# Performance work log

Hardware: AMD Instinct MI355X
Metric: run time of the kernel (lower is better)

## Reference

```python
import jax, jax.numpy as jnp
import numpy as np

EPS_IN = 1e-5   # InstanceNorm2d default eps
EPS_VAR = 1e-6  # clamp on attention variance

def instance_norm(x):
    # x: (b, c, h, w); affine=False, biased variance over spatial dims
    mean = jnp.mean(x, axis=(2, 3), keepdims=True)
    var = jnp.var(x, axis=(2, 3), keepdims=True)
    return (x - mean) * jax.lax.rsqrt(var + EPS_IN)

def setup_inputs() -> dict:
    key = jax.random.key(0)
    k1, k2, k3, k4 = jax.random.split(key, 4)
    shp = (4, 512, 64, 64)
    return {
        "c_x": jax.random.normal(k1, shp, dtype=jnp.float32),
        "s_x": jax.random.normal(k2, shp, dtype=jnp.float32),
        "c_1x": jax.random.normal(k3, shp, dtype=jnp.float32),
        "s_1x": jax.random.normal(k4, shp, dtype=jnp.float32),
    }

def reference(c_x, s_x, c_1x, s_1x):
    b, v_dim, h, w = c_x.shape
    hw = h * w
    # Q: (b, hw, qk), K: (b, qk, hw), V: (b, hw, v)
    Q = instance_norm(c_1x).reshape(b, -1, hw).transpose(0, 2, 1)
    K = instance_norm(s_1x).reshape(b, -1, s_1x.shape[2] * s_1x.shape[3])
    V = s_x.reshape(b, v_dim, -1).transpose(0, 2, 1)
    # attention over spatial tokens
    A = jax.nn.softmax(jnp.einsum('bqc,bck->bqk', Q, K), axis=-1)
    M = jnp.einsum('bqk,bkv->bqv', A, V)              # weighted mean
    Var = jnp.einsum('bqk,bkv->bqv', A, V * V) - M * M  # weighted variance
    S = jnp.sqrt(jnp.clip(Var, EPS_VAR, None))
    # back to (b, v, h, w)
    M = M.reshape(b, h, w, -1).transpose(0, 3, 1, 2)
    S = S.reshape(b, h, w, -1).transpose(0, 3, 1, 2)
    return S * instance_norm(c_x) + M
```

## Files before the change

### kernel.cpp

```cpp
#include <hip/hip_runtime.h>
#include <cmath>


#define B_  4
#define C_  512
#define HW_ 4096

typedef _Float16 f16;
typedef _Float16 f16x8 __attribute__((ext_vector_type(8)));
typedef float    f32x4 __attribute__((ext_vector_type(4)));

__device__ __forceinline__ f32x4 mfma16(f16x8 a, f16x8 b, f32x4 c) {
  return __builtin_amdgcn_mfma_f32_16x16x32_f16(a, b, c, 0, 0, 0);
}
__device__ __forceinline__ void g2l16(const f16* g, f16* l) {
  __builtin_amdgcn_global_load_lds(
      (const __attribute__((address_space(1))) void*)g,
      (__attribute__((address_space(3))) void*)l, 16, 0, 0);
}

__global__ __launch_bounds__(256) void k_stats(
    const float* __restrict__ cx, const float* __restrict__ c1,
    const float* __restrict__ s1,
    float2* __restrict__ cxs, float2* __restrict__ c1s, float2* __restrict__ s1s) {
  int c = blockIdx.x, b = blockIdx.y, t = blockIdx.z;
  const float* src = (t == 0 ? cx : (t == 1 ? c1 : s1)) + (size_t)(b * C_ + c) * HW_;
  float s = 0.f, q = 0.f;
  const float4* src4 = (const float4*)src;
  for (int i = threadIdx.x; i < HW_ / 4; i += 256) {
    float4 v = src4[i];
    s += v.x + v.y + v.z + v.w;
    q += v.x * v.x + v.y * v.y + v.z * v.z + v.w * v.w;
  }
#pragma unroll
  for (int off = 1; off < 64; off <<= 1) {
    s += __shfl_xor(s, off);
    q += __shfl_xor(q, off);
  }
  __shared__ float ss[4], sq[4];
  int wv = threadIdx.x >> 6;
  if ((threadIdx.x & 63) == 0) { ss[wv] = s; sq[wv] = q; }
  __syncthreads();
  if (threadIdx.x == 0) {
    float S = ss[0] + ss[1] + ss[2] + ss[3];
    float Q = sq[0] + sq[1] + sq[2] + sq[3];
    float mean = S * (1.f / HW_);
    float var = Q * (1.f / HW_) - mean * mean;
    float2 r;
    r.x = mean;
    r.y = rsqrtf(var + 1e-5f);
    (t == 0 ? cxs : (t == 1 ? c1s : s1s))[b * C_ + c] = r;
  }
}

__global__ __launch_bounds__(256) void k_prept(
    const float* __restrict__ src, const float2* __restrict__ st,
    f16* __restrict__ dst) {
  int pb = blockIdx.x * 64, cb = blockIdx.y * 64, b = blockIdx.z;
  __shared__ float t[64][65];
  int tj = threadIdx.x & 63, tr = threadIdx.x >> 6;
#pragma unroll 4
  for (int p = 0; p < 16; ++p) {
    int cl = p * 4 + tr;
    float2 mr = st[b * C_ + cb + cl];
    float v = src[(size_t)(b * C_ + cb + cl) * HW_ + pb + tj];
    t[cl][tj] = (v - mr.x) * mr.y;
  }
  __syncthreads();
#pragma unroll 4
  for (int p = 0; p < 16; ++p) {
    int pr = p * 4 + tr;
    dst[(size_t)(b * HW_ + pb + pr) * C_ + cb + tj] = (f16)t[tj][pr];
  }
}

__global__ __launch_bounds__(256) void k_prepv(const float* __restrict__ src,
                                               f16* __restrict__ dst) {
  int gid = blockIdx.x * 256 + threadIdx.x;
  const float4* s = (const float4*)src + (size_t)gid * 2;
  float4 v0 = s[0], v1 = s[1];
  f16x8 v = {(f16)v0.x, (f16)v0.y, (f16)v0.z, (f16)v0.w,
             (f16)v1.x, (f16)v1.y, (f16)v1.z, (f16)v1.w};
  *(f16x8*)(dst + (size_t)gid * 8) = v;
}

__global__ __launch_bounds__(256, 2) void k_qk(
    const f16* __restrict__ Qt, const f16* __restrict__ Kt,
    f16* __restrict__ E, float2* __restrict__ mlpart,
    int qspan, int qt128, int npair) {
  int id = blockIdx.x, pair, kt;
  if ((npair & 7) == 0) {
    int xcd = id & 7, j = id >> 3, qrs = npair >> 3;
    pair = xcd * qrs + (j % qrs);
    kt = j / qrs;
  } else {
    pair = id >> 4;
    kt = id & 15;
  }
  int bz = pair / qt128, qt = pair - bz * qt128;

  const f16* Aq = Qt + ((size_t)(bz * qspan + qt * 128)) * C_;
  const f16* Bk = Kt + (size_t)bz * HW_ * C_ + (size_t)kt * 256 * C_;
  f16* Eb = E + ((size_t)(bz * qspan + qt * 128)) * HW_ + kt * 256;
  float2* mlb = mlpart + ((size_t)(bz * qspan + qt * 128)) * 16 + kt;

  __shared__ __align__(16) union ShQK {
    struct { f16 As[128 * 32]; f16 Bs[256 * 32]; } s;
    f16 ebuf[32 * 272];
  } sh;
  __shared__ float sred[2][128];
  f16* As = sh.s.As;
  f16* Bs = sh.s.Bs;

  int t = threadIdx.x, wave = t >> 6, lane = t & 63, lq = lane & 15, quad = lane >> 4;
  int wy = wave >> 1, wx = wave & 1;
  int srow = t >> 2, scol = (t & 3) * 8;

  f32x4 acc[4][8];
#pragma unroll
  for (int mt = 0; mt < 4; ++mt)
#pragma unroll
    for (int nt = 0; nt < 8; ++nt) acc[mt][nt] = (f32x4){0, 0, 0, 0};

  for (int kc = 0; kc < 16; ++kc) {
    __syncthreads();
    g2l16(Aq + (size_t)srow * C_ + kc * 32 + scol, As + t * 8);
    g2l16(Aq + (size_t)(srow + 64) * C_ + kc * 32 + scol, As + 2048 + t * 8);
#pragma unroll
    for (int i = 0; i < 4; ++i)
      g2l16(Bk + (size_t)(srow + 64 * i) * C_ + kc * 32 + scol,
            Bs + i * 2048 + t * 8);
    __syncthreads();
    f16x8 af[4], bf[8];
#pragma unroll
    for (int mt = 0; mt < 4; ++mt)
      af[mt] = *(const f16x8*)(As + (wy * 64 + mt * 16 + lq) * 32 + quad * 8);
#pragma unroll
    for (int nt = 0; nt < 8; ++nt)
      bf[nt] = *(const f16x8*)(Bs + (wx * 128 + nt * 16 + lq) * 32 + quad * 8);
#pragma unroll
    for (int mt = 0; mt < 4; ++mt)
#pragma unroll
      for (int nt = 0; nt < 8; ++nt)
        acc[mt][nt] = mfma16(af[mt], bf[nt], acc[mt][nt]);
  }

#pragma unroll
  for (int mt = 0; mt < 4; ++mt)
#pragma unroll
    for (int r = 0; r < 4; ++r) {
      float v = -1e30f;
#pragma unroll
      for (int nt = 0; nt < 8; ++nt) v = fmaxf(v, acc[mt][nt][r]);
#pragma unroll
      for (int msk = 1; msk < 16; msk <<= 1) v = fmaxf(v, __shfl_xor(v, msk));
      if (lq == 0) sred[wx][wy * 64 + mt * 16 + quad * 4 + r] = v;
    }
  __syncthreads();
  float mrow[4][4];
#pragma unroll
  for (int mt = 0; mt < 4; ++mt)
#pragma unroll
    for (int r = 0; r < 4; ++r) {
      int rr = wy * 64 + mt * 16 + quad * 4 + r;
      mrow[mt][r] = fmaxf(sred[0][rr], sred[1][rr]);
    }

  float rsum[4][4];
#pragma unroll
  for (int mt = 0; mt < 4; ++mt)
#pragma unroll
    for (int r = 0; r < 4; ++r) rsum[mt][r] = 0.f;

#pragma unroll
  for (int mt = 0; mt < 4; ++mt) {
    __syncthreads();
#pragma unroll
    for (int nt = 0; nt < 8; ++nt) {
      f32x4 v = acc[mt][nt];
#pragma unroll
      for (int r = 0; r < 4; ++r) {
        float e = __expf(v[r] - mrow[mt][r]);
        rsum[mt][r] += e;
        sh.ebuf[(wy * 16 + quad * 4 + r) * 272 + wx * 128 + nt * 16 + lq] = (f16)e;
      }
    }
    __syncthreads();
#pragma unroll
    for (int i = 0; i < 4; ++i) {
      int idx = i * 256 + t;
      int rl = idx >> 5, cs = (idx & 31) * 8;
      f16x8 v8 = *(const f16x8*)(sh.ebuf + rl * 272 + cs);
      int grow = (rl >> 4) * 64 + mt * 16 + (rl & 15);
      *(f16x8*)(Eb + (size_t)grow * HW_ + cs) = v8;
    }
  }

#pragma unroll
  for (int mt = 0; mt < 4; ++mt)
#pragma unroll
    for (int r = 0; r < 4; ++r) {
      float v = rsum[mt][r];
#pragma unroll
      for (int msk = 1; msk < 16; msk <<= 1) v += __shfl_xor(v, msk);
      if (lq == 0) sred[wx][wy * 64 + mt * 16 + quad * 4 + r] = v;
    }
  __syncthreads();
  if (wx == 0 && lq == 0) {
#pragma unroll
    for (int mt = 0; mt < 4; ++mt)
#pragma unroll
      for (int r = 0; r < 4; ++r) {
        int rr = wy * 64 + mt * 16 + quad * 4 + r;
        mlb[(size_t)rr * 16] = make_float2(mrow[mt][r], sred[0][rr] + sred[1][rr]);
      }
  }
}

__global__ __launch_bounds__(256) void k_red(const float2* __restrict__ mlpart,
                                             float* __restrict__ alpha) {
  int row = blockIdx.x * 256 + threadIdx.x;
  const float2* p = mlpart + (size_t)row * 16;
  float2 loc[16];
  float m = -1e30f;
#pragma unroll
  for (int i = 0; i < 16; ++i) {
    loc[i] = p[i];
    m = fmaxf(m, loc[i].x);
  }
  float l = 0.f;
#pragma unroll
  for (int i = 0; i < 16; ++i) l += loc[i].y * __expf(loc[i].x - m);
  float invl = 1.f / l;
#pragma unroll
  for (int i = 0; i < 16; ++i)
    alpha[(size_t)row * 16 + i] = __expf(loc[i].x - m) * invl;
}

__global__ __launch_bounds__(256, 2) void k_pv(
    const f16* __restrict__ P, const float* __restrict__ alphaG,
    const f16* __restrict__ V, const float* __restrict__ cx,
    const float2* __restrict__ cxs, float* __restrict__ out,
    int qspan, int qbase, int qt128) {
  int npairs = (int)gridDim.x >> 2;
  int id = blockIdx.x, pair, ct;
  if ((npairs & 7) == 0) {
    int x = id & 7, j = id >> 3, ppx = npairs >> 3;
    pair = x * ppx + (j >> 2);
    ct = j & 3;
  } else {
    pair = id >> 2;
    ct = id & 3;
  }
  int bz = pair / qt128, qt = pair - bz * qt128;

  const f16* Ap = P + ((size_t)(bz * qspan + qt * 128)) * HW_;
  const f16* Bv = V + ((size_t)(bz * C_ + ct * 128)) * HW_;

  __shared__ __align__(16) f16 As[128 * 32], Bs[128 * 32];
  __shared__ float Al[128 * 17];

  int t = threadIdx.x, wave = t >> 6, lane = t & 63, lq = lane & 15, quad = lane >> 4;
  int wy = wave >> 1, wx = wave & 1;
  int srow = t >> 2, scol = (t & 3) * 8;

  {
    const float* ag = alphaG + ((size_t)(bz * qspan + qt * 128)) * 16;
#pragma unroll
    for (int i = 0; i < 8; ++i) {
      int e = i * 256 + t;
      Al[(e >> 4) * 17 + (e & 15)] = ag[e];
    }
  }

  f32x4 accM[4][4], accM2[4][4];
#pragma unroll
  for (int mt = 0; mt < 4; ++mt)
#pragma unroll
    for (int nt = 0; nt < 4; ++nt) {
      accM[mt][nt] = (f32x4){0, 0, 0, 0};
      accM2[mt][nt] = (f32x4){0, 0, 0, 0};
    }

  for (int kc = 0; kc < 128; ++kc) {
    __syncthreads();
    g2l16(Ap + (size_t)srow * HW_ + kc * 32 + scol, As + t * 8);
    g2l16(Ap + (size_t)(srow + 64) * HW_ + kc * 32 + scol, As + 2048 + t * 8);
    g2l16(Bv + (size_t)srow * HW_ + kc * 32 + scol, Bs + t * 8);
    g2l16(Bv + (size_t)(srow + 64) * HW_ + kc * 32 + scol, Bs + 2048 + t * 8);
    __syncthreads();

    int ktl = kc >> 3;
    f16x8 af[4], bf[4], bf2[4];
#pragma unroll
    for (int mt = 0; mt < 4; ++mt) {
      af[mt] = *(const f16x8*)(As + (wy * 64 + mt * 16 + lq) * 32 + quad * 8);
      f16 a = (f16)Al[(wy * 64 + mt * 16 + lq) * 17 + ktl];
      af[mt] = af[mt] * a;
    }
#pragma unroll
    for (int nt = 0; nt < 4; ++nt) {
      bf[nt] = *(const f16x8*)(Bs + (wx * 64 + nt * 16 + lq) * 32 + quad * 8);
      bf2[nt] = bf[nt] * bf[nt];
    }
#pragma unroll
    for (int mt = 0; mt < 4; ++mt)
#pragma unroll
      for (int nt = 0; nt < 4; ++nt) {
        accM[mt][nt] = mfma16(af[mt], bf[nt], accM[mt][nt]);
        accM2[mt][nt] = mfma16(af[mt], bf2[nt], accM2[mt][nt]);
      }
  }

  int chbase = ct * 128 + wx * 64;
#pragma unroll
  for (int mt = 0; mt < 4; ++mt) {
    int q0 = qbase + qt * 128 + wy * 64 + mt * 16 + quad * 4;
#pragma unroll
    for (int nt = 0; nt < 4; ++nt) {
      int c = chbase + nt * 16 + lq;
      float2 st = cxs[bz * C_ + c];
      size_t base = ((size_t)bz * C_ + c) * HW_ + q0;
      float4 cv = *(const float4*)(cx + base);
      f32x4 m1 = accM[mt][nt], m2 = accM2[mt][nt];
      float4 o;
      o.x = sqrtf(fmaxf(m2[0] - m1[0] * m1[0], 1e-6f)) * ((cv.x - st.x) * st.y) + m1[0];
      o.y = sqrtf(fmaxf(m2[1] - m1[1] * m1[1], 1e-6f)) * ((cv.y - st.x) * st.y) + m1[1];
      o.z = sqrtf(fmaxf(m2[2] - m1[2] * m1[2], 1e-6f)) * ((cv.z - st.x) * st.y) + m1[2];
      o.w = sqrtf(fmaxf(m2[3] - m1[3] * m1[3], 1e-6f)) * ((cv.w - st.x) * st.y) + m1[3];
      *(float4*)(out + base) = o;
    }
  }
}

extern "C" void kernel_launch(void* const* d_in, const int* in_sizes, int n_in,
                              void* d_out, int out_size, void* d_ws,
                              size_t ws_size, hipStream_t stream) {
  const float* c_x = (const float*)d_in[0];
  const float* s_x = (const float*)d_in[1];
  const float* c1x = (const float*)d_in[2];
  const float* s1x = (const float*)d_in[3];
  float* out = (float*)d_out;

  char* ws = (char*)d_ws;
  size_t o = 0;
  f16* Qt = (f16*)(ws + o);  o += (size_t)B_ * HW_ * C_ * 2;
  f16* Kt = (f16*)(ws + o);  o += (size_t)B_ * HW_ * C_ * 2;
  f16* Vh = (f16*)(ws + o);  o += (size_t)B_ * HW_ * C_ * 2;
  float2* cxs = (float2*)(ws + o); o += B_ * C_ * sizeof(float2);
  float2* c1s = (float2*)(ws + o); o += B_ * C_ * sizeof(float2);
  float2* s1s = (float2*)(ws + o); o += B_ * C_ * sizeof(float2);
  size_t fixed = (o + 255) & ~(size_t)255;

  const size_t per_row = (size_t)HW_ * 2 + 16 * 8 + 16 * 4;
  struct Cfg { int nb, qs; };
  const Cfg cfgs[5] = {{4, 4096}, {1, 4096}, {1, 2048}, {1, 1024}, {1, 512}};
  Cfg cfg = cfgs[4];
  for (int i = 0; i < 5; ++i) {
    size_t rows = (size_t)cfgs[i].nb * cfgs[i].qs;
    if (fixed + rows * per_row <= ws_size) { cfg = cfgs[i]; break; }
  }
  const int nb = cfg.nb, qspan = cfg.qs, qt128 = qspan / 128;
  const int npair = nb * qt128;
  const size_t rows = (size_t)nb * qspan;
  f16* E = (f16*)(ws + fixed);
  float2* mlpart = (float2*)(ws + fixed + rows * HW_ * 2);
  float* alpha = (float*)(ws + fixed + rows * HW_ * 2 + rows * 16 * 8);

  k_stats<<<dim3(C_, B_, 3), 256, 0, stream>>>(c_x, c1x, s1x, cxs, c1s, s1s);
  k_prept<<<dim3(HW_ / 64, C_ / 64, B_), 256, 0, stream>>>(c1x, c1s, Qt);
  k_prept<<<dim3(HW_ / 64, C_ / 64, B_), 256, 0, stream>>>(s1x, s1s, Kt);
  k_prepv<<<dim3(B_ * C_ * HW_ / 8 / 256), 256, 0, stream>>>(s_x, Vh);

  for (int b0 = 0; b0 < B_; b0 += nb) {
    for (int qb = 0; qb < HW_; qb += qspan) {
      const f16* Qtp = Qt + ((size_t)b0 * HW_ + qb) * C_;
      const f16* Ktp = Kt + (size_t)b0 * HW_ * C_;
      const f16* Vp = Vh + (size_t)b0 * C_ * HW_;
      const float* cxp = c_x + (size_t)b0 * C_ * HW_;
      const float2* cxsp = cxs + b0 * C_;
      float* outp = out + (size_t)b0 * C_ * HW_;

      k_qk<<<dim3((unsigned)(npair * 16)), 256, 0, stream>>>(
          Qtp, Ktp, E, mlpart, qspan, qt128, npair);
      k_red<<<dim3((unsigned)(rows / 256)), 256, 0, stream>>>(mlpart, alpha);
      k_pv<<<dim3((unsigned)(npair * 4)), 256, 0, stream>>>(
          E, alpha, Vp, cxp, cxsp, outp, qspan, qb, qt128);
    }
  }
}
```

Measured before the change: 428.3 us.

## Restructure PV kernel with 256x128 tiles, triple-buffered LDS and swizzle

The PV GEMM kernel moves from 128x128 tiles with 256 threads and a synchronous single-buffer K=32 loop to 256x128 tiles with 512 threads. It uses a three-stage LDS ring with K=64 steps and XOR-swizzled LDS layout. Global-to-LDS loads for stage s+2 are interleaved with MFMA phases under explicit barriers, waitcnts and setprio. Alpha is stored in LDS as fp16. The aim is to hide global load latency, cut bank conflicts and halve P/V refetching, in exchange for much higher LDS use per block, which may reduce occupancy.

```diff
diff --git a/kernel.cpp b/kernel.cpp
--- a/kernel.cpp
+++ b/kernel.cpp
@@ -237,11 +237,63 @@
     alpha[(size_t)row * 16 + i] = __expf(loc[i].x - m) * invl;
 }
 
-__global__ __launch_bounds__(256, 2) void k_pv(
+#define PV_STAGE_A(i)                                                         \
+  g2l16(Ap + (size_t)((i)*64 + srow) * HW_ + s2 * 64 + scol,                  \
+        sm + pnOff + (i)*4096 + t * 8)
+#define PV_STAGE_B(i)                                                         \
+  g2l16(Bv + (size_t)((i)*64 + srow) * HW_ + s2 * 64 + scol,                  \
+        sm + pnOff + 16384 + (i)*4096 + t * 8)
+
+#define PV_PHASE(MH, NH, STAGE_STMT, POST_STMT)                               \
+  {                                                                           \
+    f16x8 af00 = *(const f16x8*)(As_s + aoff + ((MH)*2+0)*1024 + cx0);        \
+    f16x8 af01 = *(const f16x8*)(As_s + aoff + ((MH)*2+0)*1024 + cx1);        \
+    f16x8 af10 = *(const f16x8*)(As_s + aoff + ((MH)*2+1)*1024 + cx0);        \
+    f16x8 af11 = *(const f16x8*)(As_s + aoff + ((MH)*2+1)*1024 + cx1);        \
+    f16x8 bf00 = *(const f16x8*)(Bs_s + boff + ((NH)*2+0)*1024 + cx0);        \
+    f16x8 bf01 = *(const f16x8*)(Bs_s + boff + ((NH)*2+0)*1024 + cx1);        \
+    f16x8 bf10 = *(const f16x8*)(Bs_s + boff + ((NH)*2+1)*1024 + cx0);        \
+    f16x8 bf11 = *(const f16x8*)(Bs_s + boff + ((NH)*2+1)*1024 + cx1);        \
+    STAGE_STMT;                                                               \
+    __builtin_amdgcn_s_barrier();                                             \
+    asm volatile("s_waitcnt lgkmcnt(0)" ::: "memory");                        \
+    __builtin_amdgcn_sched_barrier(0);                                        \
+    __builtin_amdgcn_s_setprio(1);                                            \
+    af00 *= aal[(MH)*2+0]; af01 *= aal[(MH)*2+0];                             \
+    af10 *= aal[(MH)*2+1]; af11 *= aal[(MH)*2+1];                             \
+    {                                                                         \
+      f16x8 b2;                                                               \
+      b2 = bf00 * bf00;                                                       \
+      accM [(MH)*2+0][(NH)*2+0] = mfma16(af00, bf00, accM [(MH)*2+0][(NH)*2+0]); \
+      accM2[(MH)*2+0][(NH)*2+0] = mfma16(af00, b2,   accM2[(MH)*2+0][(NH)*2+0]); \
+      accM [(MH)*2+1][(NH)*2+0] = mfma16(af10, bf00, accM [(MH)*2+1][(NH)*2+0]); \
+      accM2[(MH)*2+1][(NH)*2+0] = mfma16(af10, b2,   accM2[(MH)*2+1][(NH)*2+0]); \
+      b2 = bf10 * bf10;                                                       \
+      accM [(MH)*2+0][(NH)*2+1] = mfma16(af00, bf10, accM [(MH)*2+0][(NH)*2+1]); \
+      accM2[(MH)*2+0][(NH)*2+1] = mfma16(af00, b2,   accM2[(MH)*2+0][(NH)*2+1]); \
+      accM [(MH)*2+1][(NH)*2+1] = mfma16(af10, bf10, accM [(MH)*2+1][(NH)*2+1]); \
+      accM2[(MH)*2+1][(NH)*2+1] = mfma16(af10, b2,   accM2[(MH)*2+1][(NH)*2+1]); \
+      b2 = bf01 * bf01;                                                       \
+      accM [(MH)*2+0][(NH)*2+0] = mfma16(af01, bf01, accM [(MH)*2+0][(NH)*2+0]); \
+      accM2[(MH)*2+0][(NH)*2+0] = mfma16(af01, b2,   accM2[(MH)*2+0][(NH)*2+0]); \
+      accM [(MH)*2+1][(NH)*2+0] = mfma16(af11, bf01, accM [(MH)*2+1][(NH)*2+0]); \
+      accM2[(MH)*2+1][(NH)*2+0] = mfma16(af11, b2,   accM2[(MH)*2+1][(NH)*2+0]); \
+      b2 = bf11 * bf11;                                                       \
+      accM [(MH)*2+0][(NH)*2+1] = mfma16(af01, bf11, accM [(MH)*2+0][(NH)*2+1]); \
+      accM2[(MH)*2+0][(NH)*2+1] = mfma16(af01, b2,   accM2[(MH)*2+0][(NH)*2+1]); \
+      accM [(MH)*2+1][(NH)*2+1] = mfma16(af11, bf11, accM [(MH)*2+1][(NH)*2+1]); \
+      accM2[(MH)*2+1][(NH)*2+1] = mfma16(af11, b2,   accM2[(MH)*2+1][(NH)*2+1]); \
+    }                                                                         \
+    __builtin_amdgcn_s_setprio(0);                                            \
+    POST_STMT;                                                                \
+    __builtin_amdgcn_s_barrier();                                             \
+  }
+
+__global__ __launch_bounds__(512, 2) void k_pv(
     const f16* __restrict__ P, const float* __restrict__ alphaG,
     const f16* __restrict__ V, const float* __restrict__ cx,
     const float2* __restrict__ cxs, float* __restrict__ out,
-    int qspan, int qbase, int qt128) {
+    int qspan, int qbase, int qt256) {
   int npairs = (int)gridDim.x >> 2;
   int id = blockIdx.x, pair, ct;
   if ((npairs & 7) == 0) {
@@ -252,26 +304,33 @@
     pair = id >> 2;
     ct = id & 3;
   }
-  int bz = pair / qt128, qt = pair - bz * qt128;
-
-  const f16* Ap = P + ((size_t)(bz * qspan + qt * 128)) * HW_;
+  int bz = pair / qt256, qt = pair - bz * qt256;
+
+  const f16* Ap = P + ((size_t)(bz * qspan + qt * 256)) * HW_;
   const f16* Bv = V + ((size_t)(bz * C_ + ct * 128)) * HW_;
 
-  __shared__ __align__(16) f16 As[128 * 32], Bs[128 * 32];
-  __shared__ float Al[128 * 17];
+  __shared__ __align__(16) f16 sm[3 * 24576 + 256 * 17];
+  f16* Alh = sm + 3 * 24576;
 
   int t = threadIdx.x, wave = t >> 6, lane = t & 63, lq = lane & 15, quad = lane >> 4;
   int wy = wave >> 1, wx = wave & 1;
-  int srow = t >> 2, scol = (t & 3) * 8;
 
   {
-    const float* ag = alphaG + ((size_t)(bz * qspan + qt * 128)) * 16;
+    const float* ag = alphaG + ((size_t)(bz * qspan + qt * 256)) * 16;
 #pragma unroll
     for (int i = 0; i < 8; ++i) {
-      int e = i * 256 + t;
-      Al[(e >> 4) * 17 + (e & 15)] = ag[e];
-    }
-  }
+      int e = i * 512 + t;
+      Alh[(e >> 4) * 17 + (e & 15)] = (f16)ag[e];
+    }
+  }
+
+  int srow = t >> 3;
+  int scol = ((t & 7) ^ (srow & 7)) * 8;
+
+  int aoff = (wy * 64 + lq) * 64;
+  int boff = (wx * 64 + lq) * 64;
+  int cx0 = (quad * 8) ^ ((lq & 7) << 3);
+  int cx1 = (32 + quad * 8) ^ ((lq & 7) << 3);
 
   f32x4 accM[4][4], accM2[4][4];
 #pragma unroll
@@ -282,52 +341,63 @@
       accM2[mt][nt] = (f32x4){0, 0, 0, 0};
     }
 
-  for (int kc = 0; kc < 128; ++kc) {
-    __syncthreads();
-    g2l16(Ap + (size_t)srow * HW_ + kc * 32 + scol, As + t * 8);
-    g2l16(Ap + (size_t)(srow + 64) * HW_ + kc * 32 + scol, As + 2048 + t * 8);
-    g2l16(Bv + (size_t)srow * HW_ + kc * 32 + scol, Bs + t * 8);
-    g2l16(Bv + (size_t)(srow + 64) * HW_ + kc * 32 + scol, Bs + 2048 + t * 8);
-    __syncthreads();
-
-    int ktl = kc >> 3;
-    f16x8 af[4], bf[4], bf2[4];
-#pragma unroll
-    for (int mt = 0; mt < 4; ++mt) {
-      af[mt] = *(const f16x8*)(As + (wy * 64 + mt * 16 + lq) * 32 + quad * 8);
-      f16 a = (f16)Al[(wy * 64 + mt * 16 + lq) * 17 + ktl];
-      af[mt] = af[mt] * a;
-    }
-#pragma unroll
-    for (int nt = 0; nt < 4; ++nt) {
-      bf[nt] = *(const f16x8*)(Bs + (wx * 64 + nt * 16 + lq) * 32 + quad * 8);
-      bf2[nt] = bf[nt] * bf[nt];
-    }
-#pragma unroll
-    for (int mt = 0; mt < 4; ++mt)
-#pragma unroll
-      for (int nt = 0; nt < 4; ++nt) {
-        accM[mt][nt] = mfma16(af[mt], bf[nt], accM[mt][nt]);
-        accM2[mt][nt] = mfma16(af[mt], bf2[nt], accM2[mt][nt]);
-      }
+#pragma unroll
+  for (int s0 = 0; s0 < 2; ++s0) {
+    int off = s0 * 24576;
+#pragma unroll
+    for (int i = 0; i < 4; ++i)
+      g2l16(Ap + (size_t)(i * 64 + srow) * HW_ + s0 * 64 + scol,
+            sm + off + i * 4096 + t * 8);
+#pragma unroll
+    for (int i = 0; i < 2; ++i)
+      g2l16(Bv + (size_t)(i * 64 + srow) * HW_ + s0 * 64 + scol,
+            sm + off + 16384 + i * 4096 + t * 8);
+  }
+  asm volatile("s_waitcnt lgkmcnt(0)" ::: "memory");
+  asm volatile("s_waitcnt vmcnt(6)" ::: "memory");
+  __builtin_amdgcn_s_barrier();
+
+  int ph = 0, pn = 2;
+  for (int s = 0; s < 64; ++s) {
+    const f16* As_s = sm + ph * 24576;
+    const f16* Bs_s = As_s + 16384;
+    int pnOff = pn * 24576;
+    int s2 = s + 2;
+    bool st = s < 62;
+    int ktl = s >> 2;
+    f16 aal[4];
+    aal[0] = Alh[(wy * 64 + lq +  0) * 17 + ktl];
+    aal[1] = Alh[(wy * 64 + lq + 16) * 17 + ktl];
+    aal[2] = Alh[(wy * 64 + lq + 32) * 17 + ktl];
+    aal[3] = Alh[(wy * 64 + lq + 48) * 17 + ktl];
+
+    PV_PHASE(0, 0, if (st) { PV_STAGE_A(0); PV_STAGE_A(1); }, )
+    PV_PHASE(0, 1, if (st) { PV_STAGE_A(2); PV_STAGE_A(3); }, )
+    PV_PHASE(1, 0, if (st) { PV_STAGE_B(0); }, )
+    PV_PHASE(1, 1, if (st) { PV_STAGE_B(1); },
+             if (st) { asm volatile("s_waitcnt vmcnt(6)" ::: "memory"); }
+             else    { asm volatile("s_waitcnt vmcnt(0)" ::: "memory"); } )
+
+    ph = (ph == 2) ? 0 : ph + 1;
+    pn = (pn == 2) ? 0 : pn + 1;
   }
 
   int chbase = ct * 128 + wx * 64;
 #pragma unroll
   for (int mt = 0; mt < 4; ++mt) {
-    int q0 = qbase + qt * 128 + wy * 64 + mt * 16 + quad * 4;
+    int q0 = qbase + qt * 256 + wy * 64 + mt * 16 + quad * 4;
 #pragma unroll
     for (int nt = 0; nt < 4; ++nt) {
       int c = chbase + nt * 16 + lq;
-      float2 st = cxs[bz * C_ + c];
+      float2 stc = cxs[bz * C_ + c];
       size_t base = ((size_t)bz * C_ + c) * HW_ + q0;
       float4 cv = *(const float4*)(cx + base);
       f32x4 m1 = accM[mt][nt], m2 = accM2[mt][nt];
       float4 o;
-      o.x = sqrtf(fmaxf(m2[0] - m1[0] * m1[0], 1e-6f)) * ((cv.x - st.x) * st.y) + m1[0];
-      o.y = sqrtf(fmaxf(m2[1] - m1[1] * m1[1], 1e-6f)) * ((cv.y - st.x) * st.y) + m1[1];
-      o.z = sqrtf(fmaxf(m2[2] - m1[2] * m1[2], 1e-6f)) * ((cv.z - st.x) * st.y) + m1[2];
-      o.w = sqrtf(fmaxf(m2[3] - m1[3] * m1[3], 1e-6f)) * ((cv.w - st.x) * st.y) + m1[3];
+      o.x = sqrtf(fmaxf(m2[0] - m1[0] * m1[0], 1e-6f)) * ((cv.x - stc.x) * stc.y) + m1[0];
+      o.y = sqrtf(fmaxf(m2[1] - m1[1] * m1[1], 1e-6f)) * ((cv.y - stc.x) * stc.y) + m1[1];
+      o.z = sqrtf(fmaxf(m2[2] - m1[2] * m1[2], 1e-6f)) * ((cv.z - stc.x) * stc.y) + m1[2];
+      o.w = sqrtf(fmaxf(m2[3] - m1[3] * m1[3], 1e-6f)) * ((cv.w - stc.x) * stc.y) + m1[3];
       *(float4*)(out + base) = o;
     }
   }
@@ -360,8 +430,9 @@
     size_t rows = (size_t)cfgs[i].nb * cfgs[i].qs;
     if (fixed + rows * per_row <= ws_size) { cfg = cfgs[i]; break; }
   }
-  const int nb = cfg.nb, qspan = cfg.qs, qt128 = qspan / 128;
+  const int nb = cfg.nb, qspan = cfg.qs, qt128 = qspan / 128, qt256 = qspan / 256;
   const int npair = nb * qt128;
+  const int npv = nb * qt256;
   const size_t rows = (size_t)nb * qspan;
   f16* E = (f16*)(ws + fixed);
   float2* mlpart = (float2*)(ws + fixed + rows * HW_ * 2);
@@ -384,8 +455,8 @@
       k_qk<<<dim3((unsigned)(npair * 16)), 256, 0, stream>>>(
           Qtp, Ktp, E, mlpart, qspan, qt128, npair);
       k_red<<<dim3((unsigned)(rows / 256)), 256, 0, stream>>>(mlpart, alpha);
-      k_pv<<<dim3((unsigned)(npair * 4)), 256, 0, stream>>>(
-          E, alpha, Vp, cxp, cxsp, outp, qspan, qb, qt128);
-    }
-  }
-}
+      k_pv<<<dim3((unsigned)(npv * 4)), 512, 0, stream>>>(
+          E, alpha, Vp, cxp, cxsp, outp, qspan, qb, qt256);
+    }
+  }
+}
```

Result: no change. 431.8 us (+0.8%).
